# Performance work log

Hardware: AMD Instinct MI355X
Metric: run time of the kernel (lower is better)

Reference implementation:

```python
import jax, jax.numpy as jnp
import numpy as np

T, B, D, H, O = 512, 64, 512, 1024, 512

def _xavier(key, shape):
    fan_out, fan_in = shape
    limit = np.sqrt(6.0 / (fan_in + fan_out))
    return jax.random.uniform(key, shape, jnp.float32, -limit, limit)

def setup_inputs() -> dict:
    key = jax.random.key(0)
    ks = jax.random.split(key, 10)
    x = jax.random.normal(ks[0], (T, B, D), jnp.float32)
    # Gate order: i, f, o, c (stacked along first axis for a fused 4H projection;
    # math identical to 8 separate Linears in the torch module, biases init to 0
    # but we randomize them slightly for a non-trivial reference).
    Wx = jnp.concatenate([_xavier(ks[1 + g], (H, D)) for g in range(4)], axis=0)  # [4H, D]
    Wh = jnp.concatenate([_xavier(ks[5 + g], (H, H)) for g in range(4)], axis=0)  # [4H, H]
    bx = jnp.zeros((4 * H,), jnp.float32)
    bh = jnp.zeros((4 * H,), jnp.float32)
    Why = _xavier(ks[9], (O, H))
    bhy = jnp.zeros((O,), jnp.float32)
    return {"x": x, "Wx": Wx, "bx": bx, "Wh": Wh, "bh": bh, "Why": Why, "bhy": bhy}

def reference(x, Wx, bx, Wh, bh, Why, bhy):
    Hd = Wh.shape[1]
    Bd = x.shape[1]
    # Precompute all input-path projections in one batched GEMM: [T, B, 4H]
    xp = jnp.einsum('tbd,gd->tbg', x, Wx) + bx + bh

    def step(carry, xp_t):
        h, c = carry
        gates = xp_t + h @ Wh.T  # [B, 4H]
        i_t = jax.nn.sigmoid(gates[:, 0 * Hd:1 * Hd])
        f_t = jax.nn.sigmoid(gates[:, 1 * Hd:2 * Hd])
        o_t = jax.nn.sigmoid(gates[:, 2 * Hd:3 * Hd])
        c_tilde = jnp.tanh(gates[:, 3 * Hd:4 * Hd])
        c = f_t * c + i_t * c_tilde
        h = o_t * jnp.tanh(c)
        return (h, c), None

    h0 = jnp.zeros((Bd, Hd), x.dtype)
    c0 = jnp.zeros((Bd, Hd), x.dtype)
    (h, c), _ = jax.lax.scan(step, (h0, c0), xp)
    return h @ Why.T + bhy  # [B, O]
```

## Files before the change

kernel.cpp:

```cpp
#include <hip/hip_runtime.h>
#include <hip/hip_bf16.h>
#include <math.h>

constexpr int T = 512;
constexpr int B = 64;
constexpr int D = 512;
constexpr int H = 1024;
constexpr int O = 512;
constexpr int GROUPS = 2;
constexpr int BG   = B / GROUPS;
constexpr int GBLK = 128;
constexpr int COLS = 32;
constexpr int KCH  = (D + H) / 8;

typedef __attribute__((ext_vector_type(8))) __bf16 bf16x8;
typedef __attribute__((ext_vector_type(4))) float  floatx4;

struct GBar {
    unsigned arr[GBLK][32];
};

__global__ __launch_bounds__(256) void convert_w(
    const float* __restrict__ Wx, const float* __restrict__ Wh,
    __bf16* __restrict__ Wc)
{
    const int id = blockIdx.x * 256 + threadIdx.x;
    if (id >= GBLK * KCH * COLS) return;
    const int nl     = id & 31;
    const int kchunk = (id >> 5) % KCH;
    const int strip  = id / (KCH * COLS);
    const int s  = nl >> 4;
    const int jl = (nl >> 2) & 3;
    const int g  = nl & 3;
    const int j  = strip * 8 + 2 * jl + s;
    const int k0 = kchunk * 8;
    const float* src = (k0 < D) ? &Wx[(size_t)(g * H + j) * D + k0]
                                : &Wh[(size_t)(g * H + j) * H + (k0 - D)];
    const float4 a = *(const float4*)src;
    const float4 b = *(const float4*)(src + 4);
    __bf16 t8[8] = {(__bf16)a.x,(__bf16)a.y,(__bf16)a.z,(__bf16)a.w,
                    (__bf16)b.x,(__bf16)b.y,(__bf16)b.z,(__bf16)b.w};
    *(uint4*)&Wc[(size_t)id * 8] = *(uint4*)t8;
}

__global__ __launch_bounds__(256) void make_bias(
    const float* __restrict__ bx, const float* __restrict__ bh,
    float* __restrict__ bias)
{
    const int n = blockIdx.x * 256 + threadIdx.x;
    if (n < 4 * H) {
        const int gbn = n >> 5, nl = n & 31;
        const int s  = nl >> 4;
        const int jl = (nl >> 2) & 3;
        const int g  = nl & 3;
        const int j  = gbn * 8 + 2 * jl + s;
        bias[n] = bx[g * H + j] + bh[g * H + j];
    }
}

__global__ __launch_bounds__(128, 1) void lstm_persistent(
    const float* __restrict__ x,
    const __bf16* __restrict__ Wc,
    const float* __restrict__ bias,
    __bf16* __restrict__ hbufs,
    float* __restrict__ hfin,
    GBar* bars)
{
    __shared__ __attribute__((aligned(16))) __bf16 wlds[KCH * COLS * 8];

    const int tid   = threadIdx.x;
    const int wid   = tid >> 6;
    const int lane  = tid & 63;
    const int cm    = lane & 15;
    const int q     = lane >> 4;
    const int group = blockIdx.x >> 7;
    const int gb    = blockIdx.x & 127;
    const int n0    = gb * COLS;
    GBar* bar = bars + group;
    __bf16* hb0 = hbufs + (size_t)group * 2 * BG * H;
    __bf16* hb1 = hb0 + BG * H;

    {
        const uint4* wsrc = (const uint4*)(Wc + (size_t)gb * KCH * COLS * 8);
        uint4* wdst = (uint4*)wlds;
        for (int i = tid; i < KCH * COLS; i += 128) wdst[i] = wsrc[i];
    }
    const int p4 = cm & 3;
    const int jl = cm >> 2;
    const int row_l = wid * 16 + q * 4 + p4;
    const float4 bias0q = *(const float4*)&bias[n0 + jl * 4];
    const float4 bias1q = *(const float4*)&bias[n0 + 16 + jl * 4];
    float c0 = 0.f, c1 = 0.f;
    __syncthreads();

    const int grow = group * BG + wid * 16 + cm;
    const float* xrow = x + (size_t)grow * D + q * 8;
    const int    hoff = (wid * 16 + cm) * H + q * 8;
    const __bf16* wl  = wlds + (q * 32 + cm) * 8;

    floatx4 acc[2][2];
    float4  xcur[16][2];

    auto loadx = [&](int tt) {
        const float* xr = xrow + (size_t)tt * (B * D);
        #pragma unroll
        for (int s = 0; s < 16; ++s) {
            xcur[s][0] = *(const float4*)(xr + s * 32);
            xcur[s][1] = *(const float4*)(xr + s * 32 + 4);
        }
    };
    auto xmfma = [&]() {
        acc[0][0] = (floatx4){0,0,0,0}; acc[0][1] = (floatx4){0,0,0,0};
        acc[1][0] = (floatx4){0,0,0,0}; acc[1][1] = (floatx4){0,0,0,0};
        #pragma unroll
        for (int s = 0; s < 16; ++s) {
            const float4 a0 = xcur[s][0], a1 = xcur[s][1];
            const bf16x8 af = {(__bf16)a0.x,(__bf16)a0.y,(__bf16)a0.z,(__bf16)a0.w,
                               (__bf16)a1.x,(__bf16)a1.y,(__bf16)a1.z,(__bf16)a1.w};
            const bf16x8 b0 = *(const bf16x8*)(wl + s * 1024);
            const bf16x8 b1 = *(const bf16x8*)(wl + s * 1024 + 128);
            acc[0][s & 1] = __builtin_amdgcn_mfma_f32_16x16x32_bf16(af, b0, acc[0][s & 1], 0, 0, 0);
            acc[1][s & 1] = __builtin_amdgcn_mfma_f32_16x16x32_bf16(af, b1, acc[1][s & 1], 0, 0, 0);
        }
    };

    auto quadT = [&](float v[4]) {
        float w0 = __shfl_xor(v[1], 1), w1 = __shfl_xor(v[0], 1);
        float w2 = __shfl_xor(v[3], 1), w3 = __shfl_xor(v[2], 1);
        if (p4 & 1) { v[0] = w0; v[2] = w2; } else { v[1] = w1; v[3] = w3; }
        w0 = __shfl_xor(v[2], 2); w1 = __shfl_xor(v[3], 2);
        w2 = __shfl_xor(v[0], 2); w3 = __shfl_xor(v[1], 2);
        if (p4 & 2) { v[0] = w0; v[1] = w1; } else { v[2] = w2; v[3] = w3; }
    };

    loadx(0);
    xmfma();

    for (int t = 0; t < T; ++t) {
        const __bf16* hcur = (t & 1) ? hb1 : hb0;
        __bf16*       hnxt = (t & 1) ? hb0 : hb1;

        if (t > 0) {
            if (wid == 0) {
                const unsigned want = (unsigned)t;
                for (;;) {
                    const unsigned a = __hip_atomic_load(&bar->arr[2 * lane][0],
                                            __ATOMIC_RELAXED, __HIP_MEMORY_SCOPE_AGENT);
                    const unsigned b = __hip_atomic_load(&bar->arr[2 * lane + 1][0],
                                            __ATOMIC_RELAXED, __HIP_MEMORY_SCOPE_AGENT);
                    if (__ballot((a >= want) && (b >= want)) == ~0ull) break;
                    __builtin_amdgcn_s_sleep(1);
                }
            }
            __syncthreads();
        }

        {
            const __bf16* hbase = hcur + hoff;
            uint4 hv[32];
            asm volatile(
                "global_load_dwordx4 %0, %32, off sc0 sc1\n\t"
                "global_load_dwordx4 %1, %32, off offset:64 sc0 sc1\n\t"
                "global_load_dwordx4 %2, %32, off offset:128 sc0 sc1\n\t"
                "global_load_dwordx4 %3, %32, off offset:192 sc0 sc1\n\t"
                "global_load_dwordx4 %4, %32, off offset:256 sc0 sc1\n\t"
                "global_load_dwordx4 %5, %32, off offset:320 sc0 sc1\n\t"
                "global_load_dwordx4 %6, %32, off offset:384 sc0 sc1\n\t"
                "global_load_dwordx4 %7, %32, off offset:448 sc0 sc1\n\t"
                "global_load_dwordx4 %8, %32, off offset:512 sc0 sc1\n\t"
                "global_load_dwordx4 %9, %32, off offset:576 sc0 sc1\n\t"
                "global_load_dwordx4 %10, %32, off offset:640 sc0 sc1\n\t"
                "global_load_dwordx4 %11, %32, off offset:704 sc0 sc1\n\t"
                "global_load_dwordx4 %12, %32, off offset:768 sc0 sc1\n\t"
                "global_load_dwordx4 %13, %32, off offset:832 sc0 sc1\n\t"
                "global_load_dwordx4 %14, %32, off offset:896 sc0 sc1\n\t"
                "global_load_dwordx4 %15, %32, off offset:960 sc0 sc1\n\t"
                "global_load_dwordx4 %16, %32, off offset:1024 sc0 sc1\n\t"
                "global_load_dwordx4 %17, %32, off offset:1088 sc0 sc1\n\t"
                "global_load_dwordx4 %18, %32, off offset:1152 sc0 sc1\n\t"
                "global_load_dwordx4 %19, %32, off offset:1216 sc0 sc1\n\t"
                "global_load_dwordx4 %20, %32, off offset:1280 sc0 sc1\n\t"
                "global_load_dwordx4 %21, %32, off offset:1344 sc0 sc1\n\t"
                "global_load_dwordx4 %22, %32, off offset:1408 sc0 sc1\n\t"
                "global_load_dwordx4 %23, %32, off offset:1472 sc0 sc1\n\t"
                "global_load_dwordx4 %24, %32, off offset:1536 sc0 sc1\n\t"
                "global_load_dwordx4 %25, %32, off offset:1600 sc0 sc1\n\t"
                "global_load_dwordx4 %26, %32, off offset:1664 sc0 sc1\n\t"
                "global_load_dwordx4 %27, %32, off offset:1728 sc0 sc1\n\t"
                "global_load_dwordx4 %28, %32, off offset:1792 sc0 sc1\n\t"
                "global_load_dwordx4 %29, %32, off offset:1856 sc0 sc1\n\t"
                "global_load_dwordx4 %30, %32, off offset:1920 sc0 sc1\n\t"
                "global_load_dwordx4 %31, %32, off offset:1984 sc0 sc1\n\t"
                "s_waitcnt vmcnt(0)"
                : "=&v"(hv[0]),  "=&v"(hv[1]),  "=&v"(hv[2]),  "=&v"(hv[3]),
                  "=&v"(hv[4]),  "=&v"(hv[5]),  "=&v"(hv[6]),  "=&v"(hv[7]),
                  "=&v"(hv[8]),  "=&v"(hv[9]),  "=&v"(hv[10]), "=&v"(hv[11]),
                  "=&v"(hv[12]), "=&v"(hv[13]), "=&v"(hv[14]), "=&v"(hv[15]),
                  "=&v"(hv[16]), "=&v"(hv[17]), "=&v"(hv[18]), "=&v"(hv[19]),
                  "=&v"(hv[20]), "=&v"(hv[21]), "=&v"(hv[22]), "=&v"(hv[23]),
                  "=&v"(hv[24]), "=&v"(hv[25]), "=&v"(hv[26]), "=&v"(hv[27]),
                  "=&v"(hv[28]), "=&v"(hv[29]), "=&v"(hv[30]), "=&v"(hv[31])
                : "v"(hbase)
                : "memory");
            #pragma unroll
            for (int sg = 0; sg < 32; ++sg) {
                union { uint4 u; bf16x8 v; } hf; hf.u = hv[sg];
                const bf16x8 b0 = *(const bf16x8*)(wl + 16384 + sg * 1024);
                const bf16x8 b1 = *(const bf16x8*)(wl + 16384 + sg * 1024 + 128);
                acc[0][sg & 1] = __builtin_amdgcn_mfma_f32_16x16x32_bf16(hf.v, b0, acc[0][sg & 1], 0, 0, 0);
                acc[1][sg & 1] = __builtin_amdgcn_mfma_f32_16x16x32_bf16(hf.v, b1, acc[1][sg & 1], 0, 0, 0);
            }
        }
        const floatx4 av0 = acc[0][0] + acc[0][1];
        const floatx4 av1 = acc[1][0] + acc[1][1];

        float g0v[4] = {av0.x, av0.y, av0.z, av0.w};
        float g1v[4] = {av1.x, av1.y, av1.z, av1.w};
        quadT(g0v);
        quadT(g1v);

        if (t + 1 < T) loadx(t + 1);

        const float i0 = 1.f / (1.f + expf(-(g0v[0] + bias0q.x)));
        const float f0 = 1.f / (1.f + expf(-(g0v[1] + bias0q.y)));
        const float o0 = 1.f / (1.f + expf(-(g0v[2] + bias0q.z)));
        const float t0 = tanhf(g0v[3] + bias0q.w);
        const float i1 = 1.f / (1.f + expf(-(g1v[0] + bias1q.x)));
        const float f1 = 1.f / (1.f + expf(-(g1v[1] + bias1q.y)));
        const float o1 = 1.f / (1.f + expf(-(g1v[2] + bias1q.z)));
        const float t1 = tanhf(g1v[3] + bias1q.w);
        c0 = f0 * c0 + i0 * t0;
        c1 = f1 * c1 + i1 * t1;
        const float hv0 = o0 * tanhf(c0);
        const float hv1 = o1 * tanhf(c1);
        const int j0 = gb * 8 + 2 * jl;
        const int hi = row_l * H + j0;
        union { __bf16 h2[2]; unsigned u; } hp;
        hp.h2[0] = (__bf16)hv0; hp.h2[1] = (__bf16)hv1;
        __hip_atomic_store((unsigned*)&hnxt[hi], hp.u, __ATOMIC_RELAXED,
                           __HIP_MEMORY_SCOPE_AGENT);
        if (t == T - 1) {
            const int gr = group * BG + row_l;
            hfin[gr * H + j0]     = hv0;
            hfin[gr * H + j0 + 1] = hv1;
        }

        __syncthreads();

        if (tid == 0)
            __hip_atomic_store(&bar->arr[gb][0], (unsigned)(t + 1),
                               __ATOMIC_RELAXED, __HIP_MEMORY_SCOPE_AGENT);

        if (t + 1 < T) xmfma();
    }
}

__global__ __launch_bounds__(256) void out_gemm(
    const float* __restrict__ h, const float* __restrict__ Why,
    const float* __restrict__ bhy, float* __restrict__ out)
{
    const int idx = blockIdx.x * 256 + threadIdx.x;
    if (idx >= B * O) return;
    const int b = idx / O;
    const int o = idx % O;
    const float4* hv = (const float4*)&h[(size_t)b * H];
    const float4* wv = (const float4*)&Why[(size_t)o * H];
    float s = 0.f;
    #pragma unroll 4
    for (int k = 0; k < H / 4; ++k) {
        const float4 a = hv[k];
        const float4 w = wv[k];
        s += a.x * w.x + a.y * w.y + a.z * w.z + a.w * w.w;
    }
    out[idx] = s + bhy[o];
}

extern "C" void kernel_launch(void* const* d_in, const int* in_sizes, int n_in,
                              void* d_out, int out_size, void* d_ws, size_t ws_size,
                              hipStream_t stream) {
    const float* x   = (const float*)d_in[0];
    const float* Wx  = (const float*)d_in[1];
    const float* bx  = (const float*)d_in[2];
    const float* Wh  = (const float*)d_in[3];
    const float* bh  = (const float*)d_in[4];
    const float* Why = (const float*)d_in[5];
    const float* bhy = (const float*)d_in[6];
    float* out = (float*)d_out;

    char* ws = (char*)d_ws;
    __bf16* Wc    = (__bf16*)ws;
    float*  bias  = (float*)(ws + 12582912);
    __bf16* hbufs = (__bf16*)(ws + 12599296);
    GBar*   bars  = (GBar*)  (ws + 12861440);
    float*  hfin  = (float*)ws;

    (void)hipMemsetAsync(ws + 12599296, 0, 262144 + 2 * sizeof(GBar), stream);
    convert_w<<<3072, 256, 0, stream>>>(Wx, Wh, Wc);
    make_bias<<<16, 256, 0, stream>>>(bx, bh, bias);

    lstm_persistent<<<GROUPS * GBLK, 128, 0, stream>>>(x, Wc, bias, hbufs,
                                                       hfin, bars);

    out_gemm<<<(B * O + 255) / 256, 256, 0, stream>>>(hfin, Why, bhy, out);
}
```

Before: 3.243 ms.

## Replace block-wide barrier wait with per-lane chunked flag polling in h load

Removes the wave-0 spin plus __syncthreads grid barrier and instead has every lane poll the ready flags of the producer blocks for each 256-column chunk of h just before loading that chunk, so loads of early chunks can start before all blocks finish. Flags are packed contiguously instead of padded to 32 words each, so one dword load per lane covers a 32-block range. This is meant to shorten the per-step synchronization latency on the recurrent critical path. In exchange, flags now share cache lines (more contention on stores), and correctness depends on the per-lane flag-to-chunk mapping and on relaxed loads being ordered.

```diff
diff --git a/kernel.cpp b/kernel.cpp
--- a/kernel.cpp
+++ b/kernel.cpp
@@ -17,7 +17,7 @@
 typedef __attribute__((ext_vector_type(4))) float  floatx4;
 
 struct GBar {
-    unsigned arr[GBLK][32];
+    unsigned arr[GBLK];
 };
 
 __global__ __launch_bounds__(256) void convert_w(
@@ -97,6 +97,7 @@
     const float* xrow = x + (size_t)grow * D + q * 8;
     const int    hoff = (wid * 16 + cm) * H + q * 8;
     const __bf16* wl  = wlds + (q * 32 + cm) * 8;
+    const unsigned* fa = bar->arr + (lane & 31);
 
     floatx4 acc[2][2];
     float4  xcur[16][2];
@@ -140,68 +141,71 @@
         const __bf16* hcur = (t & 1) ? hb1 : hb0;
         __bf16*       hnxt = (t & 1) ? hb0 : hb1;
 
-        if (t > 0) {
-            if (wid == 0) {
-                const unsigned want = (unsigned)t;
-                for (;;) {
-                    const unsigned a = __hip_atomic_load(&bar->arr[2 * lane][0],
-                                            __ATOMIC_RELAXED, __HIP_MEMORY_SCOPE_AGENT);
-                    const unsigned b = __hip_atomic_load(&bar->arr[2 * lane + 1][0],
-                                            __ATOMIC_RELAXED, __HIP_MEMORY_SCOPE_AGENT);
-                    if (__ballot((a >= want) && (b >= want)) == ~0ull) break;
-                    __builtin_amdgcn_s_sleep(1);
-                }
-            }
-            __syncthreads();
-        }
-
         {
             const __bf16* hbase = hcur + hoff;
             uint4 hv[32];
+            unsigned ftmp;
             asm volatile(
-                "global_load_dwordx4 %0, %32, off sc0 sc1\n\t"
-                "global_load_dwordx4 %1, %32, off offset:64 sc0 sc1\n\t"
-                "global_load_dwordx4 %2, %32, off offset:128 sc0 sc1\n\t"
-                "global_load_dwordx4 %3, %32, off offset:192 sc0 sc1\n\t"
-                "global_load_dwordx4 %4, %32, off offset:256 sc0 sc1\n\t"
-                "global_load_dwordx4 %5, %32, off offset:320 sc0 sc1\n\t"
-                "global_load_dwordx4 %6, %32, off offset:384 sc0 sc1\n\t"
-                "global_load_dwordx4 %7, %32, off offset:448 sc0 sc1\n\t"
-                "global_load_dwordx4 %8, %32, off offset:512 sc0 sc1\n\t"
-                "global_load_dwordx4 %9, %32, off offset:576 sc0 sc1\n\t"
-                "global_load_dwordx4 %10, %32, off offset:640 sc0 sc1\n\t"
-                "global_load_dwordx4 %11, %32, off offset:704 sc0 sc1\n\t"
-                "global_load_dwordx4 %12, %32, off offset:768 sc0 sc1\n\t"
-                "global_load_dwordx4 %13, %32, off offset:832 sc0 sc1\n\t"
-                "global_load_dwordx4 %14, %32, off offset:896 sc0 sc1\n\t"
-                "global_load_dwordx4 %15, %32, off offset:960 sc0 sc1\n\t"
-                "global_load_dwordx4 %16, %32, off offset:1024 sc0 sc1\n\t"
-                "global_load_dwordx4 %17, %32, off offset:1088 sc0 sc1\n\t"
-                "global_load_dwordx4 %18, %32, off offset:1152 sc0 sc1\n\t"
-                "global_load_dwordx4 %19, %32, off offset:1216 sc0 sc1\n\t"
-                "global_load_dwordx4 %20, %32, off offset:1280 sc0 sc1\n\t"
-                "global_load_dwordx4 %21, %32, off offset:1344 sc0 sc1\n\t"
-                "global_load_dwordx4 %22, %32, off offset:1408 sc0 sc1\n\t"
-                "global_load_dwordx4 %23, %32, off offset:1472 sc0 sc1\n\t"
-                "global_load_dwordx4 %24, %32, off offset:1536 sc0 sc1\n\t"
-                "global_load_dwordx4 %25, %32, off offset:1600 sc0 sc1\n\t"
-                "global_load_dwordx4 %26, %32, off offset:1664 sc0 sc1\n\t"
-                "global_load_dwordx4 %27, %32, off offset:1728 sc0 sc1\n\t"
-                "global_load_dwordx4 %28, %32, off offset:1792 sc0 sc1\n\t"
-                "global_load_dwordx4 %29, %32, off offset:1856 sc0 sc1\n\t"
-                "global_load_dwordx4 %30, %32, off offset:1920 sc0 sc1\n\t"
-                "global_load_dwordx4 %31, %32, off offset:1984 sc0 sc1\n\t"
+                "1: global_load_dword %[f], %[fa], off sc0 sc1\n\t"
+                "s_waitcnt vmcnt(0)\n\t"
+                "v_cmp_gt_i32 vcc, %[tt], %[f]\n\t"
+                "s_cbranch_vccnz 1b\n\t"
+                "global_load_dwordx4 %[h0], %[hb], off sc0 sc1\n\t"
+                "global_load_dwordx4 %[h1], %[hb], off offset:64 sc0 sc1\n\t"
+                "global_load_dwordx4 %[h2], %[hb], off offset:128 sc0 sc1\n\t"
+                "global_load_dwordx4 %[h3], %[hb], off offset:192 sc0 sc1\n\t"
+                "global_load_dwordx4 %[h4], %[hb], off offset:256 sc0 sc1\n\t"
+                "global_load_dwordx4 %[h5], %[hb], off offset:320 sc0 sc1\n\t"
+                "global_load_dwordx4 %[h6], %[hb], off offset:384 sc0 sc1\n\t"
+                "global_load_dwordx4 %[h7], %[hb], off offset:448 sc0 sc1\n\t"
+                "1: global_load_dword %[f], %[fa], off offset:128 sc0 sc1\n\t"
+                "s_waitcnt vmcnt(0)\n\t"
+                "v_cmp_gt_i32 vcc, %[tt], %[f]\n\t"
+                "s_cbranch_vccnz 1b\n\t"
+                "global_load_dwordx4 %[h8], %[hb], off offset:512 sc0 sc1\n\t"
+                "global_load_dwordx4 %[h9], %[hb], off offset:576 sc0 sc1\n\t"
+                "global_load_dwordx4 %[h10], %[hb], off offset:640 sc0 sc1\n\t"
+                "global_load_dwordx4 %[h11], %[hb], off offset:704 sc0 sc1\n\t"
+                "global_load_dwordx4 %[h12], %[hb], off offset:768 sc0 sc1\n\t"
+                "global_load_dwordx4 %[h13], %[hb], off offset:832 sc0 sc1\n\t"
+                "global_load_dwordx4 %[h14], %[hb], off offset:896 sc0 sc1\n\t"
+                "global_load_dwordx4 %[h15], %[hb], off offset:960 sc0 sc1\n\t"
+                "1: global_load_dword %[f], %[fa], off offset:256 sc0 sc1\n\t"
+                "s_waitcnt vmcnt(0)\n\t"
+                "v_cmp_gt_i32 vcc, %[tt], %[f]\n\t"
+                "s_cbranch_vccnz 1b\n\t"
+                "global_load_dwordx4 %[h16], %[hb], off offset:1024 sc0 sc1\n\t"
+                "global_load_dwordx4 %[h17], %[hb], off offset:1088 sc0 sc1\n\t"
+                "global_load_dwordx4 %[h18], %[hb], off offset:1152 sc0 sc1\n\t"
+                "global_load_dwordx4 %[h19], %[hb], off offset:1216 sc0 sc1\n\t"
+                "global_load_dwordx4 %[h20], %[hb], off offset:1280 sc0 sc1\n\t"
+                "global_load_dwordx4 %[h21], %[hb], off offset:1344 sc0 sc1\n\t"
+                "global_load_dwordx4 %[h22], %[hb], off offset:1408 sc0 sc1\n\t"
+                "global_load_dwordx4 %[h23], %[hb], off offset:1472 sc0 sc1\n\t"
+                "1: global_load_dword %[f], %[fa], off offset:384 sc0 sc1\n\t"
+                "s_waitcnt vmcnt(0)\n\t"
+                "v_cmp_gt_i32 vcc, %[tt], %[f]\n\t"
+                "s_cbranch_vccnz 1b\n\t"
+                "global_load_dwordx4 %[h24], %[hb], off offset:1536 sc0 sc1\n\t"
+                "global_load_dwordx4 %[h25], %[hb], off offset:1600 sc0 sc1\n\t"
+                "global_load_dwordx4 %[h26], %[hb], off offset:1664 sc0 sc1\n\t"
+                "global_load_dwordx4 %[h27], %[hb], off offset:1728 sc0 sc1\n\t"
+                "global_load_dwordx4 %[h28], %[hb], off offset:1792 sc0 sc1\n\t"
+                "global_load_dwordx4 %[h29], %[hb], off offset:1856 sc0 sc1\n\t"
+                "global_load_dwordx4 %[h30], %[hb], off offset:1920 sc0 sc1\n\t"
+                "global_load_dwordx4 %[h31], %[hb], off offset:1984 sc0 sc1\n\t"
                 "s_waitcnt vmcnt(0)"
-                : "=&v"(hv[0]),  "=&v"(hv[1]),  "=&v"(hv[2]),  "=&v"(hv[3]),
-                  "=&v"(hv[4]),  "=&v"(hv[5]),  "=&v"(hv[6]),  "=&v"(hv[7]),
-                  "=&v"(hv[8]),  "=&v"(hv[9]),  "=&v"(hv[10]), "=&v"(hv[11]),
-                  "=&v"(hv[12]), "=&v"(hv[13]), "=&v"(hv[14]), "=&v"(hv[15]),
-                  "=&v"(hv[16]), "=&v"(hv[17]), "=&v"(hv[18]), "=&v"(hv[19]),
-                  "=&v"(hv[20]), "=&v"(hv[21]), "=&v"(hv[22]), "=&v"(hv[23]),
-                  "=&v"(hv[24]), "=&v"(hv[25]), "=&v"(hv[26]), "=&v"(hv[27]),
-                  "=&v"(hv[28]), "=&v"(hv[29]), "=&v"(hv[30]), "=&v"(hv[31])
-                : "v"(hbase)
-                : "memory");
+                : [h0]"=&v"(hv[0]),  [h1]"=&v"(hv[1]),  [h2]"=&v"(hv[2]),  [h3]"=&v"(hv[3]),
+                  [h4]"=&v"(hv[4]),  [h5]"=&v"(hv[5]),  [h6]"=&v"(hv[6]),  [h7]"=&v"(hv[7]),
+                  [h8]"=&v"(hv[8]),  [h9]"=&v"(hv[9]),  [h10]"=&v"(hv[10]), [h11]"=&v"(hv[11]),
+                  [h12]"=&v"(hv[12]), [h13]"=&v"(hv[13]), [h14]"=&v"(hv[14]), [h15]"=&v"(hv[15]),
+                  [h16]"=&v"(hv[16]), [h17]"=&v"(hv[17]), [h18]"=&v"(hv[18]), [h19]"=&v"(hv[19]),
+                  [h20]"=&v"(hv[20]), [h21]"=&v"(hv[21]), [h22]"=&v"(hv[22]), [h23]"=&v"(hv[23]),
+                  [h24]"=&v"(hv[24]), [h25]"=&v"(hv[25]), [h26]"=&v"(hv[26]), [h27]"=&v"(hv[27]),
+                  [h28]"=&v"(hv[28]), [h29]"=&v"(hv[29]), [h30]"=&v"(hv[30]), [h31]"=&v"(hv[31]),
+                  [f]"=&v"(ftmp)
+                : [hb]"v"(hbase), [fa]"v"(fa), [tt]"v"(t)
+                : "memory", "vcc");
             #pragma unroll
             for (int sg = 0; sg < 32; ++sg) {
                 union { uint4 u; bf16x8 v; } hf; hf.u = hv[sg];
@@ -248,7 +252,7 @@
         __syncthreads();
 
         if (tid == 0)
-            __hip_atomic_store(&bar->arr[gb][0], (unsigned)(t + 1),
+            __hip_atomic_store(&bar->arr[gb], (unsigned)(t + 1),
                                __ATOMIC_RELAXED, __HIP_MEMORY_SCOPE_AGENT);
 
         if (t + 1 < T) xmfma();
```

Result: slower. 3.527 ms (+8.7%).
